# Kernel tuning notes

Hardware: AMD Instinct MI355X
Metric: run time of the kernel (lower is better)

## Reference

```python
import jax, jax.numpy as jnp
import numpy as np

NUM_CLASSES = 5
SMOOTH = 1e-5


def setup_inputs() -> dict:
    key = jax.random.key(0)
    k1, k2, k3 = jax.random.split(key, 3)
    B, C, X, Y, Z = 2, NUM_CLASSES, 128, 128, 128
    net_output = jax.random.normal(k1, (B, C, X, Y, Z), dtype=jnp.float32)
    target = jax.random.randint(k2, (B, 1, X, Y, Z), 0, C, dtype=jnp.int64)
    dist = jax.random.uniform(k3, (B, 1, X, Y, Z), dtype=jnp.float32)
    return {"net_output": net_output, "target": target, "dist": dist}


def reference(net_output, target, dist):
    # --- Distance-map penalized multi-class Dice ---
    p = jax.nn.softmax(net_output, axis=1)  # (B,C,X,Y,Z)
    gt = target[:, 0]  # (B,X,Y,Z)
    classes = jnp.arange(NUM_CLASSES)[None, :, None, None, None]
    y_onehot = (gt[:, None] == classes).astype(p.dtype)  # (B,C,X,Y,Z)
    # per-class, per-batch sums over spatial dims
    tp = jnp.sum(p * y_onehot * dist, axis=(2, 3, 4))  # (B,C), dist broadcasts over C
    denom = jnp.sum(p, axis=(2, 3, 4)) + jnp.sum(y_onehot, axis=(2, 3, 4))  # (B,C)
    dc = (2.0 * tp + SMOOTH) / (denom + SMOOTH)  # (B,C)
    # sum over classes of batch-mean, divided by num_classes == overall mean
    dpdc_loss = -jnp.mean(dc)
    # --- Cross entropy (mean over all voxels), target squeezed to class idx ---
    logp = jax.nn.log_softmax(net_output, axis=1)  # (B,C,X,Y,Z)
    nll = -jnp.take_along_axis(logp, target, axis=1)  # (B,1,X,Y,Z)
    ce_loss = jnp.mean(nll)
    # aggregate == 'sum', weight_ce = weight_dice = 1
    return ce_loss + dpdc_loss
```

## Files before the change

### kernel.cpp

```cpp
#include <hip/hip_runtime.h>

#define NC 5
#define NB 2
#define SPATIAL (128*128*128)
#define NGROUPS (SPATIAL/4)
#define TILE_GROUPS 256
#define NTILES (NGROUPS/TILE_GROUPS)
#define GX 256
#define TPB (NTILES/GX)
#define SMOOTHF 1e-5f

#define TILE_BYTES (32*1024)


__device__ __forceinline__ void async16(const void* g, void* l) {
    __builtin_amdgcn_global_load_lds(
        (const __attribute__((address_space(1))) void*)g,
        (__attribute__((address_space(3))) void*)l, 16, 0, 0);
}

__global__ __launch_bounds__(256) void dpdc_main(
    const float* __restrict__ net, const void* __restrict__ targ,
    const float* __restrict__ dist, float* __restrict__ slots)
{
    __shared__ __align__(16) char lds[2][TILE_BYTES];
    const int b   = blockIdx.y;
    const int tid = threadIdx.x;

    const unsigned long long tv = ((const unsigned long long*)targ)[tid & 63];
    const int t64 = (__ballot(tv >= 5ull) == 0ull);

    const char* netb  = (const char*)net  + (size_t)b * NC * SPATIAL * 4;
    const char* distb = (const char*)dist + (size_t)b * SPATIAL * 4;
    const char* targb = (const char*)targ + (size_t)b * SPATIAL * (t64 ? 8 : 4);

    const int tl0 = blockIdx.x * TPB;

    auto stage = [&](int tl, int bf) {
        char* base = &lds[bf][0];
        const size_t toff = (size_t)tl * 4096 + tid * 16;
        #pragma unroll
        for (int c = 0; c < NC; ++c)
            async16(netb + (size_t)c * SPATIAL * 4 + toff, base + c * 4096 + tid * 16);
        async16(distb + toff, base + 20480 + tid * 16);
        if (t64) {
            const char* ts = targb + (size_t)tl * 8192 + tid * 16;
            async16(ts,        base + 24576 + tid * 16);
            async16(ts + 4096, base + 28672 + tid * 16);
        } else {
            async16(targb + toff, base + 24576 + tid * 16);
        }
    };

    float tp[NC], sp[NC], cnt[NC];
    #pragma unroll
    for (int c = 0; c < NC; ++c) { tp[c] = 0.f; sp[c] = 0.f; cnt[c] = 0.f; }
    float nll = 0.f;

    stage(tl0, 0);
    __syncthreads();

    #pragma unroll 1
    for (int k = 0; k < TPB; ++k) {
        if (k + 1 < TPB) stage(tl0 + k + 1, (k + 1) & 1);

        const char* base = &lds[k & 1][0];
        float4 l[NC];
        #pragma unroll
        for (int c = 0; c < NC; ++c)
            l[c] = *(const float4*)(base + c * 4096 + tid * 16);
        float4 dd = *(const float4*)(base + 20480 + tid * 16);
        int tt[4];
        if (t64) {
            ulonglong2 a = *(const ulonglong2*)(base + 24576 + tid * 32);
            ulonglong2 q = *(const ulonglong2*)(base + 24576 + tid * 32 + 16);
            tt[0] = (int)a.x; tt[1] = (int)a.y;
            tt[2] = (int)q.x; tt[3] = (int)q.y;
        } else {
            int4 a = *(const int4*)(base + 24576 + tid * 16);
            tt[0] = a.x; tt[1] = a.y; tt[2] = a.z; tt[3] = a.w;
        }
        const float* dv = (const float*)&dd;
        #pragma unroll
        for (int j = 0; j < 4; ++j) {
            float lc[NC];
            #pragma unroll
            for (int c = 0; c < NC; ++c) lc[c] = ((const float*)&l[c])[j];
            float m = fmaxf(fmaxf(fmaxf(lc[0], lc[1]), fmaxf(lc[2], lc[3])), lc[4]);
            float e[NC];
            float s = 0.f;
            #pragma unroll
            for (int c = 0; c < NC; ++c) { e[c] = __expf(lc[c] - m); s += e[c]; }
            float inv = 1.0f / s;
            int t = tt[j];
            float lsel = lc[4];
            #pragma unroll
            for (int c = 0; c < 4; ++c) lsel = (t == c) ? lc[c] : lsel;
            float pd = dv[j] * inv;
            #pragma unroll
            for (int c = 0; c < NC; ++c) {
                float p = e[c] * inv;
                sp[c] += p;
                tp[c] += (t == c) ? e[c] * pd : 0.f;
                cnt[c] += (t == c) ? 1.f : 0.f;
            }
            nll += __logf(s) - (lsel - m);
        }
        __syncthreads();
    }

    __shared__ float red[4][16];
    float vals[16];
    #pragma unroll
    for (int c = 0; c < NC; ++c) {
        vals[c] = tp[c]; vals[5 + c] = sp[c]; vals[10 + c] = cnt[c];
    }
    vals[15] = nll;
    const int lane = tid & 63;
    const int wave = tid >> 6;
    #pragma unroll
    for (int k = 0; k < 16; ++k) {
        float v = vals[k];
        #pragma unroll
        for (int off = 32; off > 0; off >>= 1) v += __shfl_down(v, off, 64);
        if (lane == 0) red[wave][k] = v;
    }
    __syncthreads();
    if (tid < 16) {
        float v = red[0][tid] + red[1][tid] + red[2][tid] + red[3][tid];
        slots[((size_t)b * GX + blockIdx.x) * 16 + tid] = v;
    }
}

__global__ __launch_bounds__(1024) void finalize(const float* __restrict__ slots,
                                                 float* __restrict__ out) {
    __shared__ float part[1024];
    __shared__ float tot[32];
    const int j = threadIdx.x;
    const int p = j & 31;
    const int b = p >> 4, k = p & 15;
    float s = 0.f;
    for (int slot = j >> 5; slot < GX; slot += 32)
        s += slots[((size_t)b * GX + slot) * 16 + k];
    part[j] = s;
    __syncthreads();
    if (j < 32) {
        float t = 0.f;
        #pragma unroll
        for (int m = 0; m < 32; ++m) t += part[j + 32 * m];
        tot[j] = t;
    }
    __syncthreads();
    if (j == 0) {
        float dcsum = 0.f;
        for (int bb = 0; bb < NB; ++bb)
            for (int c = 0; c < NC; ++c) {
                float tpv = tot[bb * 16 + c];
                float spv = tot[bb * 16 + 5 + c];
                float cv  = tot[bb * 16 + 10 + c];
                dcsum += (2.f * tpv + SMOOTHF) / (spv + cv + SMOOTHF);
            }
        float ce = (tot[15] + tot[31]) / (float)((size_t)NB * SPATIAL);
        out[0] = ce - dcsum / (float)(NB * NC);
    }
}

extern "C" void kernel_launch(void* const* d_in, const int* in_sizes, int n_in,
                              void* d_out, int out_size, void* d_ws, size_t ws_size,
                              hipStream_t stream) {
    const float* net  = (const float*)d_in[0];
    const void*  targ = d_in[1];
    const float* dist = (const float*)d_in[2];
    float* slots = (float*)d_ws;

    dim3 grid(GX, NB);
    dpdc_main<<<grid, 256, 0, stream>>>(net, targ, dist, slots);
    finalize<<<1, 1024, 0, stream>>>(slots, (float*)d_out);
}
```

Baseline: 33.51 us.

## Halve tile size, double grid, precompute staging pointers per thread

Shrinks each LDS tile from 1024 to 512 voxels (16KB per buffer) and doubles the grid to 512 blocks per batch, so each thread processes 2 voxels per tile instead of 4. Staging is rewritten so each thread issues up to 4 async 16-byte loads from precomputed source pointers that advance by a fixed stride. The aim is more resident blocks and better latency hiding through higher occupancy, with less address arithmetic per stage. In exchange there are more loop iterations and barriers per voxel. The grid size becomes a runtime value checked against the workspace size.

```diff
diff --git a/kernel.cpp b/kernel.cpp
--- a/kernel.cpp
+++ b/kernel.cpp
@@ -3,17 +3,14 @@
 #define NC 5
 #define NB 2
 #define SPATIAL (128*128*128)
-#define NGROUPS (SPATIAL/4)
-#define TILE_GROUPS 256
-#define NTILES (NGROUPS/TILE_GROUPS)
-#define GX 256
-#define TPB (NTILES/GX)
+#define TILE_VOX 512
+#define NTILES (SPATIAL/TILE_VOX)
 #define SMOOTHF 1e-5f
 
-#define TILE_BYTES (32*1024)
+#define TILE_BYTES (16*1024)
 
 
-__device__ __forceinline__ void async16(const void* g, void* l) {
+__device__ __forceinline__ void async16(const char* g, char* l) {
     __builtin_amdgcn_global_load_lds(
         (const __attribute__((address_space(1))) void*)g,
         (__attribute__((address_space(3))) void*)l, 16, 0, 0);
@@ -21,11 +18,10 @@
 
 __global__ __launch_bounds__(256) void dpdc_main(
     const float* __restrict__ net, const void* __restrict__ targ,
-    const float* __restrict__ dist, float* __restrict__ slots)
+    const float* __restrict__ dist, float* __restrict__ slots, int TPB)
 {
     __shared__ __align__(16) char lds[2][TILE_BYTES];
-    const int b   = blockIdx.y;
-    const int tid = threadIdx.x;
+    const int b = blockIdx.y, tid = threadIdx.x;
 
     const unsigned long long tv = ((const unsigned long long*)targ)[tid & 63];
     const int t64 = (__ballot(tv >= 5ull) == 0ull);
@@ -35,21 +31,37 @@
     const char* targb = (const char*)targ + (size_t)b * SPATIAL * (t64 ? 8 : 4);
 
     const int tl0 = blockIdx.x * TPB;
+    const int nchunk = t64 ? 1024 : 896;
 
-    auto stage = [&](int tl, int bf) {
+    const char* srcp[4];
+    int sstr[4];
+    bool act[4];
+    #pragma unroll
+    for (int k = 0; k < 4; ++k) {
+        const int q = tid + 256 * k;
+        act[k] = (q < nchunk);
+        const int r = q >> 7;
+        if (r < 5) {
+            srcp[k] = netb + (size_t)r * SPATIAL * 4
+                           + (size_t)tl0 * 2048 + (size_t)(q & 127) * 16;
+            sstr[k] = 2048;
+        } else if (r == 5) {
+            srcp[k] = distb + (size_t)tl0 * 2048 + (size_t)(q & 127) * 16;
+            sstr[k] = 2048;
+        } else {
+            const int tstr = t64 ? 4096 : 2048;
+            srcp[k] = targb + (size_t)tl0 * tstr + (size_t)(q - 768) * 16;
+            sstr[k] = tstr;
+        }
+    }
+
+    auto stage = [&](int bf) {
         char* base = &lds[bf][0];
-        const size_t toff = (size_t)tl * 4096 + tid * 16;
         #pragma unroll
-        for (int c = 0; c < NC; ++c)
-            async16(netb + (size_t)c * SPATIAL * 4 + toff, base + c * 4096 + tid * 16);
-        async16(distb + toff, base + 20480 + tid * 16);
-        if (t64) {
-            const char* ts = targb + (size_t)tl * 8192 + tid * 16;
-            async16(ts,        base + 24576 + tid * 16);
-            async16(ts + 4096, base + 28672 + tid * 16);
-        } else {
-            async16(targb + toff, base + 24576 + tid * 16);
-        }
+        for (int k = 0; k < 4; ++k)
+            if (act[k]) async16(srcp[k], base + (size_t)(tid + 256 * k) * 16);
+        #pragma unroll
+        for (int k = 0; k < 4; ++k) srcp[k] += sstr[k];
     };
 
     float tp[NC], sp[NC], cnt[NC];
@@ -57,32 +69,30 @@
     for (int c = 0; c < NC; ++c) { tp[c] = 0.f; sp[c] = 0.f; cnt[c] = 0.f; }
     float nll = 0.f;
 
-    stage(tl0, 0);
+    stage(0);
     __syncthreads();
 
     #pragma unroll 1
     for (int k = 0; k < TPB; ++k) {
-        if (k + 1 < TPB) stage(tl0 + k + 1, (k + 1) & 1);
+        if (k + 1 < TPB) stage((k + 1) & 1);
 
         const char* base = &lds[k & 1][0];
-        float4 l[NC];
+        float2 l[NC];
         #pragma unroll
         for (int c = 0; c < NC; ++c)
-            l[c] = *(const float4*)(base + c * 4096 + tid * 16);
-        float4 dd = *(const float4*)(base + 20480 + tid * 16);
-        int tt[4];
+            l[c] = *(const float2*)(base + c * 2048 + tid * 8);
+        float2 dd = *(const float2*)(base + 10240 + tid * 8);
+        int tt[2];
         if (t64) {
-            ulonglong2 a = *(const ulonglong2*)(base + 24576 + tid * 32);
-            ulonglong2 q = *(const ulonglong2*)(base + 24576 + tid * 32 + 16);
+            ulonglong2 a = *(const ulonglong2*)(base + 12288 + tid * 16);
             tt[0] = (int)a.x; tt[1] = (int)a.y;
-            tt[2] = (int)q.x; tt[3] = (int)q.y;
         } else {
-            int4 a = *(const int4*)(base + 24576 + tid * 16);
-            tt[0] = a.x; tt[1] = a.y; tt[2] = a.z; tt[3] = a.w;
+            int2 a = *(const int2*)(base + 12288 + tid * 8);
+            tt[0] = a.x; tt[1] = a.y;
         }
         const float* dv = (const float*)&dd;
         #pragma unroll
-        for (int j = 0; j < 4; ++j) {
+        for (int j = 0; j < 2; ++j) {
             float lc[NC];
             #pragma unroll
             for (int c = 0; c < NC; ++c) lc[c] = ((const float*)&l[c])[j];
@@ -128,20 +138,20 @@
     __syncthreads();
     if (tid < 16) {
         float v = red[0][tid] + red[1][tid] + red[2][tid] + red[3][tid];
-        slots[((size_t)b * GX + blockIdx.x) * 16 + tid] = v;
+        slots[((size_t)b * gridDim.x + blockIdx.x) * 16 + tid] = v;
     }
 }
 
 __global__ __launch_bounds__(1024) void finalize(const float* __restrict__ slots,
-                                                 float* __restrict__ out) {
+                                                 int gx, float* __restrict__ out) {
     __shared__ float part[1024];
     __shared__ float tot[32];
     const int j = threadIdx.x;
     const int p = j & 31;
     const int b = p >> 4, k = p & 15;
     float s = 0.f;
-    for (int slot = j >> 5; slot < GX; slot += 32)
-        s += slots[((size_t)b * GX + slot) * 16 + k];
+    for (int slot = j >> 5; slot < gx; slot += 32)
+        s += slots[((size_t)b * gx + slot) * 16 + k];
     part[j] = s;
     __syncthreads();
     if (j < 32) {
@@ -173,7 +183,11 @@
     const float* dist = (const float*)d_in[2];
     float* slots = (float*)d_ws;
 
-    dim3 grid(GX, NB);
-    dpdc_main<<<grid, 256, 0, stream>>>(net, targ, dist, slots);
-    finalize<<<1, 1024, 0, stream>>>(slots, (float*)d_out);
+    int gx = 512;
+    while ((size_t)NB * gx * 16 * sizeof(float) > ws_size && gx > 1) gx >>= 1;
+    const int tpb = NTILES / gx;
+
+    dim3 grid(gx, NB);
+    dpdc_main<<<grid, 256, 0, stream>>>(net, targ, dist, slots, tpb);
+    finalize<<<1, 1024, 0, stream>>>(slots, gx, (float*)d_out);
 }
```

Result: slower. 34.80 us (+3.9%).
